# Kernel tuning notes

Measured on AMD Instinct MI355X. Metric: run time of the kernel, lower is better.

Reference implementation:

```python
import jax, jax.numpy as jnp
import numpy as np

TARGET_SIZE = 1024
SOURCE_SIZE = 1024


def setup_inputs() -> dict:
    key = jax.random.key(0)
    k1, k2, k3, k4 = jax.random.split(key, 4)
    B, T, S = 16, 1024, 1024
    sentence_state = jax.random.normal(k1, (B, T, TARGET_SIZE), dtype=jnp.float32)
    graph_state = jax.random.normal(k2, (B, S, SOURCE_SIZE), dtype=jnp.float32)
    mask = jax.random.bernoulli(k3, 0.5, (B, T, S))  # bool
    # nn.Linear(target_size+source_size, 1, bias=False).weight flattened
    w = jax.random.normal(k4, (TARGET_SIZE + SOURCE_SIZE,), dtype=jnp.float32) * (
        1.0 / np.sqrt(TARGET_SIZE + SOURCE_SIZE)
    )
    return {"sentence_state": sentence_state, "graph_state": graph_state, "mask": mask, "w": w}


def reference(sentence_state, graph_state, mask, w):
    # Linear on concat([tgt, src]) with out_features=1 decomposes into two dot products:
    # score[b,t,s] = sentence[b,t,:] @ w_t + graph[b,s,:] @ w_s
    w_t = w[:TARGET_SIZE]
    w_s = w[TARGET_SIZE:]
    st = jnp.einsum("btd,d->bt", sentence_state, w_t)  # (B, T)
    gs = jnp.einsum("bsd,d->bs", graph_state, w_s)  # (B, S)
    scores = st[:, :, None] + gs[:, None, :]  # (B, T, S)
    attn = jax.nn.softmax(scores, axis=-1)
    attn = attn * (~mask).astype(attn.dtype)
    norm = jnp.sum(attn, axis=-1, keepdims=True) + 1e-12
    return attn / norm
```

## Files before the change

kernel.cpp:

```cpp
#include <hip/hip_runtime.h>


constexpr int Bb = 16;
constexpr int Tt = 1024;
constexpr int Ss = 1024;
constexpr int Dd = 1024;

__global__ __launch_bounds__(256) void gs_dot_kernel(
    const float* __restrict__ graph, const float* __restrict__ w_full,
    float* __restrict__ gs) {
  const int lane = threadIdx.x & 63;
  const int wv   = threadIdx.x >> 6;
  const long row = (long)blockIdx.x * 4 + wv;
  const float4* r  = reinterpret_cast<const float4*>(graph) + row * (Dd / 4);
  const float4* ws = reinterpret_cast<const float4*>(w_full + 1024);
  float acc = 0.f;
#pragma unroll
  for (int k = 0; k < 4; ++k) {
    float4 a = r[lane + 64 * k];
    float4 b = ws[lane + 64 * k];
    acc = fmaf(a.x, b.x, acc);
    acc = fmaf(a.y, b.y, acc);
    acc = fmaf(a.z, b.z, acc);
    acc = fmaf(a.w, b.w, acc);
  }
#pragma unroll
  for (int off = 32; off; off >>= 1) acc += __shfl_xor(acc, off, 64);
  if (lane == 0) gs[row] = acc;
}

__global__ __launch_bounds__(256) void softmax_probe_kernel(
    const float* __restrict__ gs, const unsigned char* __restrict__ mask,
    int* __restrict__ ws_flag, float* __restrict__ p) {
  __shared__ float redbuf[8];
  __shared__ int nz[4];
  const int tid  = threadIdx.x;
  const int lane = tid & 63;
  const int wv   = tid >> 6;
  const int b    = blockIdx.x;

  if (b == 0) {
    if (tid < 4) nz[tid] = 0;
    __syncthreads();
    uchar4 v = reinterpret_cast<const uchar4*>(mask)[tid];
    if (v.x) atomicOr(&nz[0], 1);
    if (v.y) atomicOr(&nz[1], 1);
    if (v.z) atomicOr(&nz[2], 1);
    if (v.w) atomicOr(&nz[3], 1);
    __syncthreads();
    if (tid == 0) {
      int spread = (nz[0] != 0) + (nz[1] != 0) + (nz[2] != 0) + (nz[3] != 0);
      ws_flag[0] = (spread >= 3) ? 0 : 1;
    }
  }

  float4 g = reinterpret_cast<const float4*>(gs + (long)b * Ss)[tid];
  float m = fmaxf(fmaxf(g.x, g.y), fmaxf(g.z, g.w));
#pragma unroll
  for (int off = 32; off; off >>= 1) m = fmaxf(m, __shfl_xor(m, off, 64));
  if (lane == 0) redbuf[wv] = m;
  __syncthreads();
  m = fmaxf(fmaxf(redbuf[0], redbuf[1]), fmaxf(redbuf[2], redbuf[3]));
  float4 e = make_float4(__expf(g.x - m), __expf(g.y - m),
                         __expf(g.z - m), __expf(g.w - m));
  float zs = e.x + e.y + e.z + e.w;
#pragma unroll
  for (int off = 32; off; off >>= 1) zs += __shfl_xor(zs, off, 64);
  if (lane == 0) redbuf[4 + wv] = zs;
  __syncthreads();
  const float Z    = redbuf[4] + redbuf[5] + redbuf[6] + redbuf[7];
  const float invZ = 1.0f / Z;
  reinterpret_cast<float4*>(p + (long)b * Ss)[tid] =
      make_float4(e.x * invZ, e.y * invZ, e.z * invZ, e.w * invZ);
}

__global__ __launch_bounds__(256) void PointerGenerator_9259949490200_kernel(
    const float* __restrict__ p, const unsigned char* __restrict__ mask,
    const int* __restrict__ ws_flag, float* __restrict__ out) {
  constexpr int ROWS = 8;
  const int lane = threadIdx.x & 63;
  const int wv   = threadIdx.x >> 6;
  const int b    = blockIdx.y;

  const float4* p4 = reinterpret_cast<const float4*>(p + (long)b * Ss);
  float4 pr[4];
#pragma unroll
  for (int k = 0; k < 4; ++k) pr[k] = p4[lane + 64 * k];

  const int  mode = ws_flag[0];
  const long t0   = (long)blockIdx.x * (4 * ROWS) + (long)wv * ROWS;
  const long row0 = (long)b * Tt + t0;

  unsigned int mw[ROWS][4];
  if (mode == 0) {
    const unsigned int* m4 =
        reinterpret_cast<const unsigned int*>(mask + row0 * Ss);
#pragma unroll
    for (int r = 0; r < ROWS; ++r)
#pragma unroll
      for (int k = 0; k < 4; ++k) mw[r][k] = m4[r * 256 + lane + 64 * k];
  } else {
    const int4* m4 = reinterpret_cast<const int4*>(
        reinterpret_cast<const int*>(mask) + row0 * Ss);
#pragma unroll
    for (int r = 0; r < ROWS; ++r)
#pragma unroll
      for (int k = 0; k < 4; ++k) {
        int4 w = m4[r * 256 + lane + 64 * k];
        mw[r][k] = (unsigned)(w.x != 0) | ((unsigned)(w.y != 0) << 8) |
                   ((unsigned)(w.z != 0) << 16) | ((unsigned)(w.w != 0) << 24);
      }
  }

  float sum[ROWS];
#pragma unroll
  for (int r = 0; r < ROWS; ++r) {
    float s = 0.f;
#pragma unroll
    for (int k = 0; k < 4; ++k) {
      const unsigned int m = mw[r][k];
      s += (m & 0x000000FFu) ? 0.f : pr[k].x;
      s += (m & 0x0000FF00u) ? 0.f : pr[k].y;
      s += (m & 0x00FF0000u) ? 0.f : pr[k].z;
      s += (m & 0xFF000000u) ? 0.f : pr[k].w;
    }
    sum[r] = s;
  }
#pragma unroll
  for (int off = 32; off; off >>= 1)
#pragma unroll
    for (int r = 0; r < ROWS; ++r) sum[r] += __shfl_xor(sum[r], off, 64);

#pragma unroll
  for (int r = 0; r < ROWS; ++r) {
    const float invD = 1.0f / (sum[r] + 1e-12f);
    float4* orow = reinterpret_cast<float4*>(out + (row0 + r) * Ss);
#pragma unroll
    for (int k = 0; k < 4; ++k) {
      const unsigned int m = mw[r][k];
      float4 v;
      v.x = (m & 0x000000FFu) ? 0.f : pr[k].x * invD;
      v.y = (m & 0x0000FF00u) ? 0.f : pr[k].y * invD;
      v.z = (m & 0x00FF0000u) ? 0.f : pr[k].z * invD;
      v.w = (m & 0xFF000000u) ? 0.f : pr[k].w * invD;
      orow[lane + 64 * k] = v;
    }
  }
}

extern "C" void kernel_launch(void* const* d_in, const int* in_sizes, int n_in,
                              void* d_out, int out_size, void* d_ws, size_t ws_size,
                              hipStream_t stream) {
  const float* graph        = (const float*)d_in[1];
  const unsigned char* mask = (const unsigned char*)d_in[2];
  const float* w            = (const float*)d_in[3];
  float* out = (float*)d_out;

  int*   ws_flag = (int*)d_ws;
  float* gs      = (float*)((char*)d_ws + 256);
  float* p       = gs + Bb * Ss;

  gs_dot_kernel<<<(Bb * Ss) / 4, 256, 0, stream>>>(graph, w, gs);
  softmax_probe_kernel<<<Bb, 256, 0, stream>>>(gs, mask, ws_flag, p);
  PointerGenerator_9259949490200_kernel<<<dim3(Tt / (4 * 8), Bb), 256, 0, stream>>>(
      p, mask, ws_flag, out);
}
```

Baseline: 38.33 us.

## Fold softmax normalization into masked renormalization and drop the softmax kernel

Because the output is renormalized by the masked row sum, the softmax's max-subtraction and partition-function division cancel out. The first kernel now writes exp(gs) directly and also performs the mask-layout probe, so the 16-block softmax launch and its global round-trip disappear. Rows per wave in the output kernel drop from 8 to 2, giving more blocks and lower register pressure. Without max-subtraction, exp can overflow for large scores, and the 1e-12 epsilon now acts on an unscaled sum, so correctness relies on scores staying moderate.

Result: faster. 35.85 us, median of 3 (-6.5%).

```diff
diff --git a/kernel.cpp b/kernel.cpp
--- a/kernel.cpp
+++ b/kernel.cpp
@@ -6,9 +6,27 @@
 constexpr int Ss = 1024;
 constexpr int Dd = 1024;
 
-__global__ __launch_bounds__(256) void gs_dot_kernel(
+__global__ __launch_bounds__(256) void gs_exp_probe_kernel(
     const float* __restrict__ graph, const float* __restrict__ w_full,
-    float* __restrict__ gs) {
+    const unsigned char* __restrict__ mask, int* __restrict__ ws_flag,
+    float* __restrict__ e_out) {
+  if (blockIdx.x == 0) {
+    __shared__ int nz[4];
+    const int tid = threadIdx.x;
+    if (tid < 4) nz[tid] = 0;
+    __syncthreads();
+    uchar4 v = reinterpret_cast<const uchar4*>(mask)[tid];
+    if (v.x) atomicOr(&nz[0], 1);
+    if (v.y) atomicOr(&nz[1], 1);
+    if (v.z) atomicOr(&nz[2], 1);
+    if (v.w) atomicOr(&nz[3], 1);
+    __syncthreads();
+    if (tid == 0) {
+      int spread = (nz[0] != 0) + (nz[1] != 0) + (nz[2] != 0) + (nz[3] != 0);
+      ws_flag[0] = (spread >= 3) ? 0 : 1;
+    }
+  }
+
   const int lane = threadIdx.x & 63;
   const int wv   = threadIdx.x >> 6;
   const long row = (long)blockIdx.x * 4 + wv;
@@ -26,66 +44,21 @@
   }
 #pragma unroll
   for (int off = 32; off; off >>= 1) acc += __shfl_xor(acc, off, 64);
-  if (lane == 0) gs[row] = acc;
-}
-
-__global__ __launch_bounds__(256) void softmax_probe_kernel(
-    const float* __restrict__ gs, const unsigned char* __restrict__ mask,
-    int* __restrict__ ws_flag, float* __restrict__ p) {
-  __shared__ float redbuf[8];
-  __shared__ int nz[4];
-  const int tid  = threadIdx.x;
-  const int lane = tid & 63;
-  const int wv   = tid >> 6;
-  const int b    = blockIdx.x;
-
-  if (b == 0) {
-    if (tid < 4) nz[tid] = 0;
-    __syncthreads();
-    uchar4 v = reinterpret_cast<const uchar4*>(mask)[tid];
-    if (v.x) atomicOr(&nz[0], 1);
-    if (v.y) atomicOr(&nz[1], 1);
-    if (v.z) atomicOr(&nz[2], 1);
-    if (v.w) atomicOr(&nz[3], 1);
-    __syncthreads();
-    if (tid == 0) {
-      int spread = (nz[0] != 0) + (nz[1] != 0) + (nz[2] != 0) + (nz[3] != 0);
-      ws_flag[0] = (spread >= 3) ? 0 : 1;
-    }
-  }
-
-  float4 g = reinterpret_cast<const float4*>(gs + (long)b * Ss)[tid];
-  float m = fmaxf(fmaxf(g.x, g.y), fmaxf(g.z, g.w));
-#pragma unroll
-  for (int off = 32; off; off >>= 1) m = fmaxf(m, __shfl_xor(m, off, 64));
-  if (lane == 0) redbuf[wv] = m;
-  __syncthreads();
-  m = fmaxf(fmaxf(redbuf[0], redbuf[1]), fmaxf(redbuf[2], redbuf[3]));
-  float4 e = make_float4(__expf(g.x - m), __expf(g.y - m),
-                         __expf(g.z - m), __expf(g.w - m));
-  float zs = e.x + e.y + e.z + e.w;
-#pragma unroll
-  for (int off = 32; off; off >>= 1) zs += __shfl_xor(zs, off, 64);
-  if (lane == 0) redbuf[4 + wv] = zs;
-  __syncthreads();
-  const float Z    = redbuf[4] + redbuf[5] + redbuf[6] + redbuf[7];
-  const float invZ = 1.0f / Z;
-  reinterpret_cast<float4*>(p + (long)b * Ss)[tid] =
-      make_float4(e.x * invZ, e.y * invZ, e.z * invZ, e.w * invZ);
+  if (lane == 0) e_out[row] = __expf(acc);
 }
 
 __global__ __launch_bounds__(256) void PointerGenerator_9259949490200_kernel(
-    const float* __restrict__ p, const unsigned char* __restrict__ mask,
+    const float* __restrict__ e, const unsigned char* __restrict__ mask,
     const int* __restrict__ ws_flag, float* __restrict__ out) {
-  constexpr int ROWS = 8;
+  constexpr int ROWS = 2;
   const int lane = threadIdx.x & 63;
   const int wv   = threadIdx.x >> 6;
   const int b    = blockIdx.y;
 
-  const float4* p4 = reinterpret_cast<const float4*>(p + (long)b * Ss);
+  const float4* e4 = reinterpret_cast<const float4*>(e + (long)b * Ss);
   float4 pr[4];
 #pragma unroll
-  for (int k = 0; k < 4; ++k) pr[k] = p4[lane + 64 * k];
+  for (int k = 0; k < 4; ++k) pr[k] = e4[lane + 64 * k];
 
   const int  mode = ws_flag[0];
   const long t0   = (long)blockIdx.x * (4 * ROWS) + (long)wv * ROWS;
@@ -157,11 +130,10 @@
   float* out = (float*)d_out;
 
   int*   ws_flag = (int*)d_ws;
-  float* gs      = (float*)((char*)d_ws + 256);
-  float* p       = gs + Bb * Ss;
+  float* e       = (float*)((char*)d_ws + 256);
 
-  gs_dot_kernel<<<(Bb * Ss) / 4, 256, 0, stream>>>(graph, w, gs);
-  softmax_probe_kernel<<<Bb, 256, 0, stream>>>(gs, mask, ws_flag, p);
-  PointerGenerator_9259949490200_kernel<<<dim3(Tt / (4 * 8), Bb), 256, 0, stream>>>(
-      p, mask, ws_flag, out);
+  gs_exp_probe_kernel<<<(Bb * Ss) / 4, 256, 0, stream>>>(graph, w, mask,
+                                                         ws_flag, e);
+  PointerGenerator_9259949490200_kernel<<<dim3(Tt / (4 * 2), Bb), 256, 0, stream>>>(
+      e, mask, ws_flag, out);
 }
```
